# Kernel tuning notes

Hardware: AMD Instinct MI355X
Metric: run time of the kernel (lower is better)

The kernel has to match this reference:

```python
import jax, jax.numpy as jnp
import numpy as np

N_USERS = 100000
N_ITEMS = 200000
N_NODES = N_USERS + N_ITEMS
EMB_DIM = 64
N_EDGES = 4000000
N_LAYERS = 2
BATCH = 8192
EMB_REG = 2.5e-5


def setup_inputs() -> dict:
    key = jax.random.key(0)
    k = jax.random.split(key, 7)
    return {
        "user_emb": jax.random.normal(k[0], (N_USERS, EMB_DIM), jnp.float32) * 0.1,
        "item_emb": jax.random.normal(k[1], (N_ITEMS, EMB_DIM), jnp.float32) * 0.1,
        "all_h": jax.random.randint(k[2], (N_EDGES,), 0, N_NODES, jnp.int64 if jax.config.jax_enable_x64 else jnp.int32),
        "all_t": jax.random.randint(k[3], (N_EDGES,), 0, N_NODES, jnp.int64 if jax.config.jax_enable_x64 else jnp.int32),
        "users": jax.random.randint(k[4], (BATCH,), 0, N_USERS),
        "pos_items": jax.random.randint(k[5], (BATCH,), 0, N_ITEMS),
        "neg_items": jax.random.randint(k[6], (BATCH,), 0, N_ITEMS),
    }


def _spmm(h, t, vals, x):
    # out[h] += vals * x[t]  over all edges; [N_NODES, D]
    return jax.ops.segment_sum(vals[:, None] * x[t], h, num_segments=N_NODES)


def reference(user_emb, item_emb, all_h, all_t, users, pos_items, neg_items):
    # symmetric normalization G = D^{-1/2} A D^{-1/2} on the edge list
    deg = jax.ops.segment_sum(jnp.ones((all_h.shape[0],), user_emb.dtype), all_h,
                              num_segments=N_NODES)
    dinv = jnp.where(deg > 0, deg ** -0.5, 0.0)
    g_vals = dinv[all_h] * dinv[all_t]

    # inference1: n_layers of SpMM with residual; sum over all layer outputs
    # (dropout p=0 on the main branch in the source -> identity)
    emb = jnp.concatenate([user_emb, item_emb], axis=0)  # [N, D]
    acc = emb
    for _ in range(N_LAYERS):
        emb = _spmm(all_h, all_t, g_vals, emb) + emb
        acc = acc + emb
    ua, ia = acc[:N_USERS], acc[N_USERS:]

    # BPR loss on the batch
    u = ua[users]
    pos = ia[pos_items]
    neg = ia[neg_items]
    pos_scores = jnp.sum(u * pos, axis=1)
    neg_scores = jnp.sum(u * neg, axis=1)
    mf_loss = jnp.mean(jax.nn.softplus(neg_scores - pos_scores))

    # embedding L2 regularization on the pre-propagation embeddings
    u_pre = user_emb[users]
    pos_pre = item_emb[pos_items]
    neg_pre = item_emb[neg_items]
    emb_loss = EMB_REG * (jnp.sum(u_pre ** 2) + jnp.sum(pos_pre ** 2)
                          + jnp.sum(neg_pre ** 2))
    return (mf_loss, emb_loss)
```

## Files before the change

kernel.cpp:

```cpp
#include <hip/hip_runtime.h>
#include <math.h>

#define N_USERS 100000
#define N_ITEMS 200000
#define N_NODES 300000
#define EMB_DIM 64
#define N_EDGES 4000000
#define BATCH   8192
#define EMB_REG 2.5e-05f

#define BUCK_SH 9
#define BN      512
#define NBUCK   586
#define BSLOT   7424
#define EPB     8192
#define EPT     32
#define NBLK_A  489
#define NBLK_MARK (BATCH / 256)
#define PACK_SH 19
#define SCORE_BLOCKS (BATCH / 4)

typedef unsigned short u16;
typedef unsigned int   u32;
typedef unsigned char  u8;
typedef __attribute__((ext_vector_type(8))) u16 u16x8;
typedef __attribute__((ext_vector_type(2))) float f32x2;

__device__ __forceinline__ float bf2f(u16 x) {
    u32 u = ((u32)x) << 16;
    return __builtin_bit_cast(float, u);
}
__device__ __forceinline__ u16 f2bf(float f) {
    u32 u = __builtin_bit_cast(u32, f);
    return (u16)((u + 0x7FFFu + ((u >> 16) & 1u)) >> 16);
}

__global__ __launch_bounds__(256) void kA(const int* __restrict__ hh,
                                          const int* __restrict__ tt,
                                          int* __restrict__ bcur, int* __restrict__ gp,
                                          const int* __restrict__ users,
                                          const int* __restrict__ pos,
                                          const int* __restrict__ neg,
                                          u8* __restrict__ flags,
                                          u8* __restrict__ e0s8) {
    if (blockIdx.x >= NBLK_A) {
        int i = (blockIdx.x - NBLK_A) * 256 + threadIdx.x;
        if (i < BATCH) {
            flags[users[i]] = 1;
            flags[N_USERS + pos[i]] = 1;
            flags[N_USERS + neg[i]] = 1;
        }
        if (blockIdx.x == NBLK_A && threadIdx.x < 16)
            ((int*)(e0s8 + (size_t)N_NODES * EMB_DIM))[threadIdx.x] = 0;
        return;
    }
    __shared__ int sh_cnt[NBUCK];
    __shared__ int sh_off[NBUCK];
    __shared__ int sh_base[NBUCK];
    __shared__ int stage[EPB];
    __shared__ u16 sbid[EPB];
    int tid = threadIdx.x;
    for (int j = tid; j < NBUCK; j += 256) sh_cnt[j] = 0;
    __syncthreads();
    int cbase = blockIdx.x * EPB;
    int clen  = min(EPB, N_EDGES - cbase);
    int pk[EPT], bk[EPT];
    #pragma unroll
    for (int j = 0; j < EPT; ++j) {
        int i = j * 256 + tid;
        bk[j] = -1;
        if (i < clen) {
            int h = hh[cbase + i];
            int t = tt[cbase + i];
            int b = h >> BUCK_SH;
            bk[j] = b;
            pk[j] = ((h & (BN - 1)) << PACK_SH) | t;
            atomicAdd(&sh_cnt[b], 1);
        }
    }
    __syncthreads();
    if (tid < 64) {
        int lane = tid, carry = 0;
        for (int b0 = 0; b0 < NBUCK; b0 += 64) {
            int idx = b0 + lane;
            int v = (idx < NBUCK) ? sh_cnt[idx] : 0;
            int incl = v;
            #pragma unroll
            for (int d = 1; d < 64; d <<= 1) {
                int u = __shfl_up(incl, d, 64);
                if (lane >= d) incl += u;
            }
            if (idx < NBUCK) sh_off[idx] = carry + incl - v;
            carry += __shfl(incl, 63, 64);
        }
    }
    __syncthreads();
    for (int j = tid; j < NBUCK; j += 256) {
        int c = sh_cnt[j];
        sh_base[j] = j * BSLOT + (c ? atomicAdd(&bcur[j], c) : 0);
        sh_cnt[j] = 0;
    }
    __syncthreads();
    #pragma unroll
    for (int j = 0; j < EPT; ++j) {
        if (bk[j] >= 0) {
            int r = atomicAdd(&sh_cnt[bk[j]], 1);
            int p = sh_off[bk[j]] + r;
            stage[p] = pk[j];
            sbid[p]  = (u16)bk[j];
        }
    }
    __syncthreads();
    for (int i = tid; i < clen; i += 256) {
        int b = sbid[i];
        gp[sh_base[b] + i - sh_off[b]] = stage[i];
    }
}

__global__ __launch_bounds__(256) void kB(const int* __restrict__ bcur,
                                          int* __restrict__ gp,
                                          int2* __restrict__ sde, float* __restrict__ dinv,
                                          const float* __restrict__ uemb,
                                          const float* __restrict__ iemb,
                                          u8* __restrict__ e0s8) {
    __shared__ int   ncnt[BN];
    __shared__ int   noff[BN];
    __shared__ float sdv[BN];
    __shared__ int   slots[BSLOT];
    int b = blockIdx.x;
    int node0 = b << BUCK_SH;
    int nn = min(BN, N_NODES - node0);
    int base = b * BSLOT;
    int count = bcur[b];
    int tid = threadIdx.x;
    for (int j = tid; j < BN; j += 256) ncnt[j] = 0;
    __syncthreads();
    for (int i = tid; i < count; i += 256)
        atomicAdd(&ncnt[gp[base + i] >> PACK_SH], 1);
    __syncthreads();
    if (tid < 64) {
        int lane = tid, carry = 0;
        #pragma unroll
        for (int b0 = 0; b0 < BN; b0 += 64) {
            int idx = b0 + lane;
            int v = ncnt[idx];
            int incl = v;
            #pragma unroll
            for (int d = 1; d < 64; d <<= 1) {
                int u = __shfl_up(incl, d, 64);
                if (lane >= d) incl += u;
            }
            noff[idx] = carry + incl - v;
            carry += __shfl(incl, 63, 64);
        }
    }
    __syncthreads();
    for (int j = tid; j < nn; j += 256) {
        int c = ncnt[j];
        float dv = c > 0 ? rsqrtf((float)c) : 0.0f;
        sde[node0 + j]  = make_int2(base + noff[j], c);
        dinv[node0 + j] = dv;
        sdv[j] = dv;
    }
    __syncthreads();
    for (int j = tid; j < BN; j += 256) ncnt[j] = noff[j];
    __syncthreads();
    for (int i = tid; i < count; i += 256) {
        int p = gp[base + i];
        int r = atomicAdd(&ncnt[p >> PACK_SH], 1);
        slots[r] = p & ((1 << PACK_SH) - 1);
    }
    __syncthreads();
    for (int i = tid; i < count; i += 256)
        gp[base + i] = slots[i];
    for (int i = tid; i < nn * 8; i += 256) {
        int j = i >> 3;
        float sc = sdv[j];
        int gnode = node0 + j;
        size_t ebase = (size_t)gnode * EMB_DIM + (size_t)(i & 7) * 8;
        const size_t UELEMS = (size_t)N_USERS * EMB_DIM;
        const float* src = (ebase < UELEMS) ? uemb + ebase : iemb + (ebase - UELEMS);
        float4 a  = ((const float4*)src)[0];
        float4 c4 = ((const float4*)src)[1];
        u32 w0 = __builtin_amdgcn_cvt_pk_fp8_f32(sc * a.x,  sc * a.y,  0,  false);
        w0 = __builtin_amdgcn_cvt_pk_fp8_f32(sc * a.z,  sc * a.w,  w0, true);
        u32 w1 = __builtin_amdgcn_cvt_pk_fp8_f32(sc * c4.x, sc * c4.y, 0,  false);
        w1 = __builtin_amdgcn_cvt_pk_fp8_f32(sc * c4.z, sc * c4.w, w1, true);
        uint2 o; o.x = w0; o.y = w1;
        ((uint2*)e0s8)[(size_t)gnode * 8 + (i & 7)] = o;
    }
}

__global__ __launch_bounds__(256) void k_spmm1(const int2* __restrict__ sde,
                        const int* __restrict__ et,
                        const u8* __restrict__ src8,
                        const float* __restrict__ uemb, const float* __restrict__ iemb,
                        const u8* __restrict__ flags,
                        u16* __restrict__ dstb, u8* __restrict__ dst8) {
    int lane = threadIdx.x & 63;
    int g    = lane >> 2;
    int sl   = lane & 3;
    int gb   = lane & 60;
    int node = blockIdx.x * 64 + ((threadIdx.x >> 6) << 4) + g;
    bool alive = node < N_NODES;
    int2 se = alive ? sde[node] : make_int2(0, 0);
    int s = se.x, ne = se.y;
    float dh = ne > 0 ? rsqrtf((float)ne) : 0.0f;
    float acc[16];
    #pragma unroll
    for (int k = 0; k < 16; ++k) acc[k] = 0.f;
    int nb = (ne + 3) & ~3;
    for (int j0 = 0; j0 < nb; j0 += 4) {
        int idx = j0 + sl;
        int ets = (idx < ne) ? et[s + idx] : N_NODES;
        #pragma unroll
        for (int jj = 0; jj < 4; ++jj) {
            int t = __shfl(ets, gb | jj, 64);
            uint4 d8 = ((const uint4*)(src8 + (size_t)t * EMB_DIM))[sl];
            f32x2 p;
            p = __builtin_amdgcn_cvt_pk_f32_fp8(d8.x, false); acc[0]  += p.x; acc[1]  += p.y;
            p = __builtin_amdgcn_cvt_pk_f32_fp8(d8.x, true);  acc[2]  += p.x; acc[3]  += p.y;
            p = __builtin_amdgcn_cvt_pk_f32_fp8(d8.y, false); acc[4]  += p.x; acc[5]  += p.y;
            p = __builtin_amdgcn_cvt_pk_f32_fp8(d8.y, true);  acc[6]  += p.x; acc[7]  += p.y;
            p = __builtin_amdgcn_cvt_pk_f32_fp8(d8.z, false); acc[8]  += p.x; acc[9]  += p.y;
            p = __builtin_amdgcn_cvt_pk_f32_fp8(d8.z, true);  acc[10] += p.x; acc[11] += p.y;
            p = __builtin_amdgcn_cvt_pk_f32_fp8(d8.w, false); acc[12] += p.x; acc[13] += p.y;
            p = __builtin_amdgcn_cvt_pk_f32_fp8(d8.w, true);  acc[14] += p.x; acc[15] += p.y;
        }
    }
    if (!alive) return;
    const float* srow = (node < N_USERS)
        ? uemb + (size_t)node * EMB_DIM
        : iemb + (size_t)(node - N_USERS) * EMB_DIM;
    float4 a0 = ((const float4*)srow)[sl * 4 + 0];
    float4 a1 = ((const float4*)srow)[sl * 4 + 1];
    float4 a2 = ((const float4*)srow)[sl * 4 + 2];
    float4 a3 = ((const float4*)srow)[sl * 4 + 3];
    float v[16];
    v[0]  = dh * acc[0]  + a0.x; v[1]  = dh * acc[1]  + a0.y;
    v[2]  = dh * acc[2]  + a0.z; v[3]  = dh * acc[3]  + a0.w;
    v[4]  = dh * acc[4]  + a1.x; v[5]  = dh * acc[5]  + a1.y;
    v[6]  = dh * acc[6]  + a1.z; v[7]  = dh * acc[7]  + a1.w;
    v[8]  = dh * acc[8]  + a2.x; v[9]  = dh * acc[9]  + a2.y;
    v[10] = dh * acc[10] + a2.z; v[11] = dh * acc[11] + a2.w;
    v[12] = dh * acc[12] + a3.x; v[13] = dh * acc[13] + a3.y;
    v[14] = dh * acc[14] + a3.z; v[15] = dh * acc[15] + a3.w;
    uint4 ow;
    u32 w;
    w = __builtin_amdgcn_cvt_pk_fp8_f32(dh * v[0],  dh * v[1],  0, false);
    w = __builtin_amdgcn_cvt_pk_fp8_f32(dh * v[2],  dh * v[3],  w, true);  ow.x = w;
    w = __builtin_amdgcn_cvt_pk_fp8_f32(dh * v[4],  dh * v[5],  0, false);
    w = __builtin_amdgcn_cvt_pk_fp8_f32(dh * v[6],  dh * v[7],  w, true);  ow.y = w;
    w = __builtin_amdgcn_cvt_pk_fp8_f32(dh * v[8],  dh * v[9],  0, false);
    w = __builtin_amdgcn_cvt_pk_fp8_f32(dh * v[10], dh * v[11], w, true);  ow.z = w;
    w = __builtin_amdgcn_cvt_pk_fp8_f32(dh * v[12], dh * v[13], 0, false);
    w = __builtin_amdgcn_cvt_pk_fp8_f32(dh * v[14], dh * v[15], w, true);  ow.w = w;
    ((uint4*)(dst8 + (size_t)node * EMB_DIM))[sl] = ow;
    if (flags[node]) {
        u16x8 o0, o1;
        o0.s0 = f2bf(v[0]);  o0.s1 = f2bf(v[1]);  o0.s2 = f2bf(v[2]);  o0.s3 = f2bf(v[3]);
        o0.s4 = f2bf(v[4]);  o0.s5 = f2bf(v[5]);  o0.s6 = f2bf(v[6]);  o0.s7 = f2bf(v[7]);
        o1.s0 = f2bf(v[8]);  o1.s1 = f2bf(v[9]);  o1.s2 = f2bf(v[10]); o1.s3 = f2bf(v[11]);
        o1.s4 = f2bf(v[12]); o1.s5 = f2bf(v[13]); o1.s6 = f2bf(v[14]); o1.s7 = f2bf(v[15]);
        ((u16x8*)(dstb + (size_t)node * EMB_DIM))[sl * 2]     = o0;
        ((u16x8*)(dstb + (size_t)node * EMB_DIM))[sl * 2 + 1] = o1;
    }
}

__global__ void k_score(const int* __restrict__ users, const int* __restrict__ pos,
                        const int* __restrict__ neg,
                        const float* __restrict__ uemb, const float* __restrict__ iemb,
                        const u16* __restrict__ emb1b, const u8* __restrict__ emb1s8,
                        const int2* __restrict__ sde, const int* __restrict__ et,
                        const float* __restrict__ dinv,
                        float* __restrict__ pmf, float* __restrict__ psq) {
    __shared__ float smf[4], ssq[4];
    int gid = blockIdx.x * blockDim.x + threadIdx.x;
    int b = gid >> 6;
    int d = gid & 63;
    int w = threadIdx.x >> 6;
    int u  = users[b];
    int pi = pos[b];
    int ni = neg[b];
    int nodes[3];
    nodes[0] = u; nodes[1] = N_USERS + pi; nodes[2] = N_USERS + ni;
    float pre[3];
    pre[0] = uemb[(size_t)u * EMB_DIM + d];
    pre[1] = iemb[(size_t)pi * EMB_DIM + d];
    pre[2] = iemb[(size_t)ni * EMB_DIM + d];
    int s0[3], ne[3], ets[3];
    float dv[3];
    #pragma unroll
    for (int k = 0; k < 3; ++k) {
        int v = nodes[k];
        int2 se = sde[v];
        s0[k] = se.x; ne[k] = se.y;
        dv[k] = dinv[v];
        ets[k] = (d < ne[k]) ? et[se.x + d] : 0;
    }
    float a[3];
    #pragma unroll
    for (int k = 0; k < 3; ++k) {
        float ac = 0.f;
        int lim = ne[k] < 64 ? ne[k] : 64;
        for (int j = 0; j < lim; ++j) {
            int t = __shfl(ets[k], j, 64);
            u32 byte = emb1s8[(size_t)t * EMB_DIM + d];
            ac += __builtin_amdgcn_cvt_f32_fp8(byte, 0);
        }
        for (int i = s0[k] + 64; i < s0[k] + ne[k]; ++i) {
            int t = et[i];
            u32 byte = emb1s8[(size_t)t * EMB_DIM + d];
            ac += __builtin_amdgcn_cvt_f32_fp8(byte, 0);
        }
        a[k] = pre[k] + 2.0f * bf2f(emb1b[(size_t)nodes[k] * EMB_DIM + d]) + dv[k] * ac;
    }
    float ps = a[0] * a[1];
    float ns = a[0] * a[2];
    float sq = pre[0] * pre[0] + pre[1] * pre[1] + pre[2] * pre[2];
    #pragma unroll
    for (int off2 = 32; off2 > 0; off2 >>= 1) {
        ps += __shfl_down(ps, off2, 64);
        ns += __shfl_down(ns, off2, 64);
        sq += __shfl_down(sq, off2, 64);
    }
    if (d == 0) {
        float x  = ns - ps;
        smf[w] = fmaxf(x, 0.0f) + log1pf(expf(-fabsf(x)));
        ssq[w] = sq;
    }
    __syncthreads();
    if (threadIdx.x == 0) {
        pmf[blockIdx.x] = smf[0] + smf[1] + smf[2] + smf[3];
        psq[blockIdx.x] = ssq[0] + ssq[1] + ssq[2] + ssq[3];
    }
}

__global__ void k_final(const float* __restrict__ pmf, const float* __restrict__ psq,
                        float* __restrict__ out) {
    __shared__ float smf[4], ssq[4];
    int tid = threadIdx.x;
    float mf = 0.f, sq = 0.f;
    #pragma unroll
    for (int i = 0; i < SCORE_BLOCKS / 256; ++i) {
        mf += pmf[tid + i * 256];
        sq += psq[tid + i * 256];
    }
    #pragma unroll
    for (int off2 = 32; off2 > 0; off2 >>= 1) {
        mf += __shfl_down(mf, off2, 64);
        sq += __shfl_down(sq, off2, 64);
    }
    if ((tid & 63) == 0) { smf[tid >> 6] = mf; ssq[tid >> 6] = sq; }
    __syncthreads();
    if (tid == 0) {
        out[0] = (smf[0] + smf[1] + smf[2] + smf[3]) * (1.0f / BATCH);
        out[1] = EMB_REG * (ssq[0] + ssq[1] + ssq[2] + ssq[3]);
    }
}

extern "C" void kernel_launch(void* const* d_in, const int* in_sizes, int n_in,
                              void* d_out, int out_size, void* d_ws, size_t ws_size,
                              hipStream_t stream) {
    const float* uemb  = (const float*)d_in[0];
    const float* iemb  = (const float*)d_in[1];
    const int*   all_h = (const int*)d_in[2];
    const int*   all_t = (const int*)d_in[3];
    const int*   users = (const int*)d_in[4];
    const int*   pos   = (const int*)d_in[5];
    const int*   neg   = (const int*)d_in[6];
    float* out = (float*)d_out;

    int*   ws     = (int*)d_ws;
    float* dinv   = (float*)ws;
    int2*  sde    = (int2*)(ws + 300032);
    u8*    flags  = (u8*)(ws + 900096);
    int*   bcur   = ws + 975104;
    float* pmf    = (float*)(ws + 976128);
    float* psq    = (float*)(ws + 978176);
    int*   gp     = ws + 980224;
    u8*    e0s8   = (u8*)(ws + 5330688);
    u8*    emb1s8 = (u8*)(ws + 10130944);
    u16*   emb1b  = (u16*)(ws + 14930944);

    hipMemsetAsync(flags, 0, 304128, stream);

    kA <<<NBLK_A + NBLK_MARK, 256, 0, stream>>>(all_h, all_t, bcur, gp,
                                                users, pos, neg, flags, e0s8);
    kB <<<NBUCK, 256, 0, stream>>>(bcur, gp, sde, dinv, uemb, iemb, e0s8);

    k_spmm1<<<(N_NODES + 63) / 64, 256, 0, stream>>>(sde, gp, e0s8, uemb, iemb,
                                                     flags, emb1b, emb1s8);

    k_score<<<SCORE_BLOCKS, 256, 0, stream>>>(users, pos, neg, uemb, iemb,
                                              emb1b, emb1s8, sde, gp, dinv, pmf, psq);
    k_final<<<1, 256, 0, stream>>>(pmf, psq, out);
}
```

Baseline: 289.6 us.

## Fuse final reduction into score kernel, split SpMM launch, reset flags in-kernel

Removes the separate k_final launch by having the last k_score block, chosen by an atomic counter, do the global reduction. The large flags memset is replaced by a small memset of bcur/cnt, and the flags are cleared inside k_score for the next call. k_spmm1 is split into two half launches and writes a zero sentinel row at N_NODES, so k_score's gather loop can be unrolled by 4 with padded indices. Together these cut launch and memset overhead and add memory-level parallelism in k_score, at the cost of an extra launch and reliance on the flags being zero on the first call.

```diff
diff --git a/kernel.cpp b/kernel.cpp
--- a/kernel.cpp
+++ b/kernel.cpp
@@ -19,6 +19,7 @@
 #define NBLK_MARK (BATCH / 256)
 #define PACK_SH 19
 #define SCORE_BLOCKS (BATCH / 4)
+#define SPMM_HALF 2344
 
 typedef unsigned short u16;
 typedef unsigned int   u32;
@@ -196,12 +197,13 @@
                         const u8* __restrict__ src8,
                         const float* __restrict__ uemb, const float* __restrict__ iemb,
                         const u8* __restrict__ flags,
-                        u16* __restrict__ dstb, u8* __restrict__ dst8) {
+                        u16* __restrict__ dstb, u8* __restrict__ dst8,
+                        int node_base) {
     int lane = threadIdx.x & 63;
     int g    = lane >> 2;
     int sl   = lane & 3;
     int gb   = lane & 60;
-    int node = blockIdx.x * 64 + ((threadIdx.x >> 6) << 4) + g;
+    int node = node_base + blockIdx.x * 64 + ((threadIdx.x >> 6) << 4) + g;
     bool alive = node < N_NODES;
     int2 se = alive ? sde[node] : make_int2(0, 0);
     int s = se.x, ne = se.y;
@@ -228,7 +230,13 @@
             p = __builtin_amdgcn_cvt_pk_f32_fp8(d8.w, true);  acc[14] += p.x; acc[15] += p.y;
         }
     }
-    if (!alive) return;
+    if (!alive) {
+        if (node == N_NODES) {
+            uint4 z; z.x = 0; z.y = 0; z.z = 0; z.w = 0;
+            ((uint4*)(dst8 + (size_t)N_NODES * EMB_DIM))[sl] = z;
+        }
+        return;
+    }
     const float* srow = (node < N_USERS)
         ? uemb + (size_t)node * EMB_DIM
         : iemb + (size_t)(node - N_USERS) * EMB_DIM;
@@ -273,8 +281,11 @@
                         const u16* __restrict__ emb1b, const u8* __restrict__ emb1s8,
                         const int2* __restrict__ sde, const int* __restrict__ et,
                         const float* __restrict__ dinv,
-                        float* __restrict__ pmf, float* __restrict__ psq) {
+                        float* __restrict__ pmf, float* __restrict__ psq,
+                        u8* __restrict__ flags, int* __restrict__ cnt,
+                        float* __restrict__ out) {
     __shared__ float smf[4], ssq[4];
+    __shared__ int swin;
     int gid = blockIdx.x * blockDim.x + threadIdx.x;
     int b = gid >> 6;
     int d = gid & 63;
@@ -296,17 +307,27 @@
         int2 se = sde[v];
         s0[k] = se.x; ne[k] = se.y;
         dv[k] = dinv[v];
-        ets[k] = (d < ne[k]) ? et[se.x + d] : 0;
+        ets[k] = (d < ne[k]) ? et[se.x + d] : N_NODES;
     }
     float a[3];
     #pragma unroll
     for (int k = 0; k < 3; ++k) {
         float ac = 0.f;
         int lim = ne[k] < 64 ? ne[k] : 64;
-        for (int j = 0; j < lim; ++j) {
-            int t = __shfl(ets[k], j, 64);
-            u32 byte = emb1s8[(size_t)t * EMB_DIM + d];
-            ac += __builtin_amdgcn_cvt_f32_fp8(byte, 0);
+        int lim4 = (lim + 3) & ~3;
+        for (int j = 0; j < lim4; j += 4) {
+            int t0 = __shfl(ets[k], j,     64);
+            int t1 = __shfl(ets[k], j + 1, 64);
+            int t2 = __shfl(ets[k], j + 2, 64);
+            int t3 = __shfl(ets[k], j + 3, 64);
+            u32 b0 = emb1s8[(size_t)t0 * EMB_DIM + d];
+            u32 b1 = emb1s8[(size_t)t1 * EMB_DIM + d];
+            u32 b2 = emb1s8[(size_t)t2 * EMB_DIM + d];
+            u32 b3 = emb1s8[(size_t)t3 * EMB_DIM + d];
+            ac += __builtin_amdgcn_cvt_f32_fp8(b0, 0);
+            ac += __builtin_amdgcn_cvt_f32_fp8(b1, 0);
+            ac += __builtin_amdgcn_cvt_f32_fp8(b2, 0);
+            ac += __builtin_amdgcn_cvt_f32_fp8(b3, 0);
         }
         for (int i = s0[k] + 64; i < s0[k] + ne[k]; ++i) {
             int t = et[i];
@@ -329,33 +350,46 @@
         smf[w] = fmaxf(x, 0.0f) + log1pf(expf(-fabsf(x)));
         ssq[w] = sq;
     }
+    {
+        int* fi = (int*)flags;
+        int idx = blockIdx.x * 37 + threadIdx.x;
+        if (threadIdx.x < 37 && idx < (N_NODES + 3) / 4 + 8)
+            fi[idx] = 0;
+    }
     __syncthreads();
     if (threadIdx.x == 0) {
         pmf[blockIdx.x] = smf[0] + smf[1] + smf[2] + smf[3];
         psq[blockIdx.x] = ssq[0] + ssq[1] + ssq[2] + ssq[3];
-    }
-}
-
-__global__ void k_final(const float* __restrict__ pmf, const float* __restrict__ psq,
-                        float* __restrict__ out) {
-    __shared__ float smf[4], ssq[4];
-    int tid = threadIdx.x;
-    float mf = 0.f, sq = 0.f;
-    #pragma unroll
-    for (int i = 0; i < SCORE_BLOCKS / 256; ++i) {
-        mf += pmf[tid + i * 256];
-        sq += psq[tid + i * 256];
-    }
-    #pragma unroll
-    for (int off2 = 32; off2 > 0; off2 >>= 1) {
-        mf += __shfl_down(mf, off2, 64);
-        sq += __shfl_down(sq, off2, 64);
-    }
-    if ((tid & 63) == 0) { smf[tid >> 6] = mf; ssq[tid >> 6] = sq; }
-    __syncthreads();
-    if (tid == 0) {
-        out[0] = (smf[0] + smf[1] + smf[2] + smf[3]) * (1.0f / BATCH);
-        out[1] = EMB_REG * (ssq[0] + ssq[1] + ssq[2] + ssq[3]);
+        __threadfence();
+        int old = __hip_atomic_fetch_add(cnt, 1, __ATOMIC_ACQ_REL,
+                                         __HIP_MEMORY_SCOPE_AGENT);
+        swin = (old == SCORE_BLOCKS - 1) ? 1 : 0;
+    }
+    __syncthreads();
+    if (swin) {
+        __threadfence();
+        int tid = threadIdx.x;
+        float mf = 0.f, sq2 = 0.f;
+        #pragma unroll
+        for (int i = 0; i < SCORE_BLOCKS / 256; ++i) {
+            u32 um = __hip_atomic_load((const u32*)&pmf[tid + i * 256],
+                                       __ATOMIC_RELAXED, __HIP_MEMORY_SCOPE_AGENT);
+            u32 us = __hip_atomic_load((const u32*)&psq[tid + i * 256],
+                                       __ATOMIC_RELAXED, __HIP_MEMORY_SCOPE_AGENT);
+            mf += __builtin_bit_cast(float, um);
+            sq2 += __builtin_bit_cast(float, us);
+        }
+        #pragma unroll
+        for (int off2 = 32; off2 > 0; off2 >>= 1) {
+            mf += __shfl_down(mf, off2, 64);
+            sq2 += __shfl_down(sq2, off2, 64);
+        }
+        if ((tid & 63) == 0) { smf[tid >> 6] = mf; ssq[tid >> 6] = sq2; }
+        __syncthreads();
+        if (tid == 0) {
+            out[0] = (smf[0] + smf[1] + smf[2] + smf[3]) * (1.0f / BATCH);
+            out[1] = EMB_REG * (ssq[0] + ssq[1] + ssq[2] + ssq[3]);
+        }
     }
 }
 
@@ -382,17 +416,20 @@
     u8*    e0s8   = (u8*)(ws + 5330688);
     u8*    emb1s8 = (u8*)(ws + 10130944);
     u16*   emb1b  = (u16*)(ws + 14930944);
-
-    hipMemsetAsync(flags, 0, 304128, stream);
+    int*   cnt    = bcur + 640;
+
+    hipMemsetAsync(bcur, 0, 4096, stream);
 
     kA <<<NBLK_A + NBLK_MARK, 256, 0, stream>>>(all_h, all_t, bcur, gp,
                                                 users, pos, neg, flags, e0s8);
     kB <<<NBUCK, 256, 0, stream>>>(bcur, gp, sde, dinv, uemb, iemb, e0s8);
 
-    k_spmm1<<<(N_NODES + 63) / 64, 256, 0, stream>>>(sde, gp, e0s8, uemb, iemb,
-                                                     flags, emb1b, emb1s8);
+    k_spmm1<<<SPMM_HALF, 256, 0, stream>>>(sde, gp, e0s8, uemb, iemb,
+                                           flags, emb1b, emb1s8, 0);
+    k_spmm1<<<SPMM_HALF, 256, 0, stream>>>(sde, gp, e0s8, uemb, iemb,
+                                           flags, emb1b, emb1s8, SPMM_HALF * 64);
 
     k_score<<<SCORE_BLOCKS, 256, 0, stream>>>(users, pos, neg, uemb, iemb,
-                                              emb1b, emb1s8, sde, gp, dinv, pmf, psq);
-    k_final<<<1, 256, 0, stream>>>(pmf, psq, out);
-}
+                                              emb1b, emb1s8, sde, gp, dinv,
+                                              pmf, psq, flags, cnt, out);
+}
```

Measured after the change: 362.9 us. 25.3% more time.
